# Kernel tuning notes

Hardware: AMD Instinct MI355X
Metric: run time of the kernel (lower is better)

Reference implementation:

```python
import jax, jax.numpy as jnp
import numpy as np

HEADS = 8
DIM_HEAD = 64
CHUNK = 128
EPS = 1e-6
KERNEL_EPS = 1e-4


def softmax_kernel(x, proj, is_query):
    # x: [b,h,n,d], proj: [f,d]  (FAVOR+ positive softmax features)
    d = x.shape[-1]
    data_normalizer = d ** -0.25
    ratio = proj.shape[0] ** -0.5
    data_dash = jnp.einsum('bhnd,fd->bhnf', x * data_normalizer, proj)
    diag = 0.5 * (data_normalizer ** 2) * jnp.sum(x * x, axis=-1, keepdims=True)  # [b,h,n,1]
    if is_query:
        m = jnp.max(data_dash, axis=-1, keepdims=True)
    else:
        m = jnp.max(data_dash, axis=(-1, -2), keepdims=True)
    return ratio * (jnp.exp(data_dash - diag - jax.lax.stop_gradient(m)) + KERNEL_EPS)


def infer_hidden_states(q, k, v, chunk_size=CHUNK):
    # q,k: [b,h,n,f], v: [b,h,n,e]; chunked causal linear attention with carried cumsums
    b, h, n, f = q.shape
    e = v.shape[-1]
    nc = n // chunk_size

    def to_chunks(t):
        return jnp.moveaxis(t.reshape(b, h, nc, chunk_size, t.shape[-1]), 2, 0)

    qs, ks, vs = to_chunks(q), to_chunks(k), to_chunks(v)

    def step(carry, inp):
        Z, S = carry  # [b,h,1,f], [b,h,1,f,e]
        qc, kc, vc = inp
        k_cum = Z + jnp.cumsum(kc, axis=2)                       # [b,h,c,f]
        D_inv = 1.0 / jnp.einsum('bhnf,bhnf->bhn', qc, k_cum + EPS)
        ctx = jnp.einsum('bhnf,bhne->bhnfe', kc, vc)             # [b,h,c,f,e]
        ctx_cum = S + jnp.cumsum(ctx, axis=2)
        out = jnp.einsum('bhnfe,bhnf,bhn->bhne', ctx_cum, qc, D_inv)
        return (k_cum[:, :, -1:], ctx_cum[:, :, -1:]), out

    init = (jnp.zeros((b, h, 1, f), q.dtype), jnp.zeros((b, h, 1, f, e), q.dtype))
    (Z, S), outs = jax.lax.scan(step, init, (qs, ks, vs))
    out = jnp.moveaxis(outs, 0, 2).reshape(b, h, n, e)
    return out, Z[:, :, 0], S[:, :, 0]


def reference(x, proj, Wq, Wk, Wv, Wo, bo):
    b, n, dim = x.shape
    h, dh = HEADS, DIM_HEAD

    def split_heads(t):
        return jnp.transpose(t.reshape(b, n, h, dh), (0, 2, 1, 3))

    q = split_heads(x @ Wq)
    k = split_heads(x @ Wk)
    v = split_heads(x @ Wv)

    qf = softmax_kernel(q, proj, is_query=True)
    kf = softmax_kernel(k, proj, is_query=False)

    out, Z, S = infer_hidden_states(qf, kf, v)
    out = jnp.transpose(out, (0, 2, 1, 3)).reshape(b, n, h * dh)
    out = out @ Wo + bo
    return out, Z, S


def setup_inputs() -> dict:
    key = jax.random.key(0)
    ks = jax.random.split(key, 6)
    b, n, dim = 2, 2048, 512
    f = 256
    return {
        'x': jax.random.normal(ks[0], (b, n, dim), jnp.float32),
        'proj': jax.random.normal(ks[1], (f, DIM_HEAD), jnp.float32),
        'Wq': jax.random.normal(ks[2], (dim, dim), jnp.float32) * (dim ** -0.5),
        'Wk': jax.random.normal(ks[3], (dim, dim), jnp.float32) * (dim ** -0.5),
        'Wv': jax.random.normal(ks[4], (dim, dim), jnp.float32) * (dim ** -0.5),
        'Wo': jax.random.normal(ks[5], (dim, dim), jnp.float32) * (dim ** -0.5),
        'bo': jnp.zeros((dim,), jnp.float32),
    }
```

## Files before the change

kernel.cpp:

```cpp
#include <hip/hip_runtime.h>
#include <hip/hip_bf16.h>
#include <math.h>

#define NB    2
#define NSEQ  2048
#define DIMM  512
#define NH    8
#define DHd   64
#define FF    256
#define CHK   128
#define NCHK  16
#define NBH   16

typedef unsigned short ushort_t;
typedef __attribute__((ext_vector_type(8))) __bf16 bf16x8;
typedef __attribute__((ext_vector_type(4))) float floatx4;

__device__ __forceinline__ unsigned short f2bf(float x) {
    union { __hip_bfloat16 h; unsigned short u; } v;
    v.h = __float2bfloat16(x);
    return v.u;
}
__device__ __forceinline__ float bf2f(unsigned short u) {
    union { unsigned short u2[2]; float f; } v;
    v.u2[0] = 0; v.u2[1] = u;
    return v.f;
}
__device__ __forceinline__ unsigned enc_f(float x) {
    unsigned u = __float_as_uint(x);
    return (u & 0x80000000u) ? ~u : (u | 0x80000000u);
}
__device__ __forceinline__ float dec_f(unsigned e) {
    unsigned u = (e & 0x80000000u) ? (e & 0x7fffffffu) : ~e;
    return __uint_as_float(u);
}

__device__ __forceinline__ void gload16(const void* g, void* l) {
    __builtin_amdgcn_global_load_lds(
        (const __attribute__((address_space(1))) void*)g,
        (__attribute__((address_space(3))) void*)l, 16, 0, 0);
}

__device__ __forceinline__ bf16x8 frag8(const ushort_t* lds, int row, int kb) {
    return *((const bf16x8*)lds + row * 8 + (kb ^ (row & 7)));
}
__device__ __forceinline__ bf16x8 fragS(const ushort_t* lds, int row, int kb) {
    return *((const bf16x8*)lds + row * 16 + (kb ^ (row & 15)));
}

__global__ __launch_bounds__(256)
void prep(const float* __restrict__ x, const float* __restrict__ proj,
          const float* __restrict__ W0, const float* __restrict__ W1,
          const float* __restrict__ W2, const float* __restrict__ W3,
          ushort_t* __restrict__ xb, ushort_t* __restrict__ projb,
          ushort_t* __restrict__ T0, ushort_t* __restrict__ T1,
          ushort_t* __restrict__ T2, ushort_t* __restrict__ T3,
          unsigned* __restrict__ mk_u)
{
    __shared__ float t[32][33];
    const int b = blockIdx.x, tid = threadIdx.x;
    if (b < 2048) {
        const int gid = b * 256 + tid;
        const float4 v = *(const float4*)(x + (size_t)gid * 4);
        union { ushort4 v4; unsigned short s[4]; } pk;
        pk.s[0] = f2bf(v.x); pk.s[1] = f2bf(v.y); pk.s[2] = f2bf(v.z); pk.s[3] = f2bf(v.w);
        ((ushort4*)xb)[gid] = pk.v4;
    } else if (b < 2064) {
        const int gid = (b - 2048) * 256 + tid;
        const float dn = 0.35355339059327379f;
        const float4 v = *(const float4*)(proj + (size_t)gid * 4);
        union { ushort4 v4; unsigned short s[4]; } pk;
        pk.s[0] = f2bf(v.x * dn); pk.s[1] = f2bf(v.y * dn);
        pk.s[2] = f2bf(v.z * dn); pk.s[3] = f2bf(v.w * dn);
        ((ushort4*)projb)[gid] = pk.v4;
    } else if (b < 3088) {
        const int idx = b - 2064;
        const int z = idx >> 8, rem = idx & 255;
        const int bx = rem & 15, by = rem >> 4;
        const float* W = (z == 0) ? W0 : (z == 1) ? W1 : (z == 2) ? W2 : W3;
        ushort_t* T = (z == 0) ? T0 : (z == 1) ? T1 : (z == 2) ? T2 : T3;
        const int x0 = bx * 32, y0 = by * 32;
        const int tx = tid & 31, ty = tid >> 5;
#pragma unroll
        for (int i = 0; i < 4; i++)
            t[ty + i * 8][tx] = W[(size_t)(y0 + ty + i * 8) * DIMM + x0 + tx];
        __syncthreads();
#pragma unroll
        for (int i = 0; i < 4; i++)
            T[(size_t)(x0 + ty + i * 8) * DIMM + y0 + tx] = f2bf(t[tx][ty + i * 8]);
    } else {
        if (tid < NBH) mk_u[tid] = 0u;
    }
}

__device__ __forceinline__ void mfma_mainloop(
    const ushort_t* __restrict__ AG, const ushort_t* __restrict__ BG,
    ushort_t* As, ushort_t* Bs, int ldA, int ldB, int K,
    floatx4 acc[4][4], int tid)
{
    const int lane = tid & 63, wid = tid >> 6;
    const int q = lane >> 4, c = lane & 15;
    const int wm = (wid >> 1) * 64, wn = (wid & 1) * 64;

    for (int k0 = 0; k0 < K; k0 += 64) {
#pragma unroll
        for (int t = 0; t < 4; t++) {
            const int g = t * 256 + tid, r = g >> 3, kb = (g & 7) ^ (r & 7);
            gload16(AG + (size_t)r * ldA + k0 + kb * 8, As + (size_t)g * 8);
        }
#pragma unroll
        for (int t = 0; t < 4; t++) {
            const int g = t * 256 + tid, r = g >> 3, kb = (g & 7) ^ (r & 7);
            gload16(BG + (size_t)r * ldB + k0 + kb * 8, Bs + (size_t)g * 8);
        }
        __syncthreads();
#pragma unroll
        for (int ks = 0; ks < 2; ks++) {
            bf16x8 af[4], bfr[4];
#pragma unroll
            for (int i = 0; i < 4; i++) {
                af[i]  = frag8(As, wm + i * 16 + c, ks * 4 + q);
                bfr[i] = frag8(Bs, wn + i * 16 + c, ks * 4 + q);
            }
#pragma unroll
            for (int i = 0; i < 4; i++)
#pragma unroll
                for (int j = 0; j < 4; j++)
                    acc[i][j] = __builtin_amdgcn_mfma_f32_16x16x32_bf16(
                        af[i], bfr[j], acc[i][j], 0, 0, 0);
        }
        __syncthreads();
    }
}

__global__ __launch_bounds__(256)
void gemm_qkv(const ushort_t* __restrict__ xb,
              const ushort_t* __restrict__ Wtq, const ushort_t* __restrict__ Wtk,
              const ushort_t* __restrict__ Wtv, const ushort_t* __restrict__ projb,
              ushort_t* __restrict__ qb, ushort_t* __restrict__ kb,
              ushort_t* __restrict__ vTb, unsigned* __restrict__ mk_u)
{
    __shared__ alignas(16) ushort_t SM[25600];
    __shared__ float red[256];
    ushort_t* As = SM;
    ushort_t* Bs = SM + 8192;
    ushort_t* PS = SM + 17408;
    const int tid = threadIdx.x;
    const int n0 = blockIdx.x * 128, m0 = blockIdx.y * 128, z = blockIdx.z;
    const ushort_t* Bt = (z == 0) ? Wtq : ((z == 1) ? Wtk : Wtv);

    floatx4 zero = {0.f, 0.f, 0.f, 0.f};
    floatx4 acc[4][4];
#pragma unroll
    for (int i = 0; i < 4; i++)
#pragma unroll
        for (int j = 0; j < 4; j++) acc[i][j] = zero;

    mfma_mainloop(xb + (size_t)m0 * DIMM, Bt + (size_t)n0 * DIMM, As, Bs,
                  DIMM, DIMM, DIMM, acc, tid);

    const int lane = tid & 63, wid = tid >> 6;
    const int q = lane >> 4, cl = lane & 15;
    const int wm = (wid >> 1) * 64, wn = (wid & 1) * 64;

#pragma unroll
    for (int i = 0; i < 4; i++)
#pragma unroll
        for (int j = 0; j < 4; j++) {
            const int col = wn + j * 16 + cl;
#pragma unroll
            for (int r = 0; r < 4; r++) {
                const int row = wm + i * 16 + q * 4 + r;
                SM[row * 136 + col] = f2bf(acc[i][j][r]);
            }
        }
    __syncthreads();

    if (z < 2) {
        ushort_t* ob = (z == 0) ? qb : kb;
        if (z == 1) {
#pragma unroll
            for (int t = 0; t < 4; t++) {
                const int g = t * 256 + tid, f = g >> 3, kbg = (g & 7) ^ (f & 7);
                gload16(projb + (size_t)f * 64 + kbg * 8, PS + (size_t)g * 8);
            }
        }
#pragma unroll
        for (int p = 0; p < 16; p++) {
            const int idx = p * 256 + tid;
            const int row = idx >> 5, c4 = idx & 31;
            ushort4 o = *(const ushort4*)&SM[row * 136 + c4 * 4];
            *(ushort4*)(ob + (size_t)(m0 + row) * DIMM + n0 + c4 * 4) = o;
        }
        if (z == 1) {
            const int bb = m0 >> 11;
            const int h0 = n0 >> 6;
            float mx[2] = {-3.0e38f, -3.0e38f};
#pragma unroll
            for (int half = 0; half < 2; half++) {
                __syncthreads();
#pragma unroll
                for (int hh = 0; hh < 2; hh++) {
                    floatx4 a2[4][4];
#pragma unroll
                    for (int i = 0; i < 4; i++)
#pragma unroll
                        for (int j = 0; j < 4; j++) a2[i][j] = zero;
#pragma unroll
                    for (int ks = 0; ks < 2; ks++) {
                        bf16x8 af[4], bfr[4];
#pragma unroll
                        for (int i = 0; i < 4; i++)
                            af[i] = *(const bf16x8*)&SM[(wm + i * 16 + cl) * 136 + hh * 64 + (ks * 4 + q) * 8];
#pragma unroll
                        for (int j = 0; j < 4; j++)
                            bfr[j] = frag8(PS, wn + j * 16 + cl, ks * 4 + q);
#pragma unroll
                        for (int i = 0; i < 4; i++)
#pragma unroll
                            for (int j = 0; j < 4; j++)
                                a2[i][j] = __builtin_amdgcn_mfma_f32_16x16x32_bf16(
                                    af[i], bfr[j], a2[i][j], 0, 0, 0);
                    }
#pragma unroll
                    for (int i = 0; i < 4; i++)
#pragma unroll
                        for (int j = 0; j < 4; j++)
#pragma unroll
                            for (int r = 0; r < 4; r++) mx[hh] = fmaxf(mx[hh], a2[i][j][r]);
                }
                if (half == 0) {
                    __syncthreads();
#pragma unroll
                    for (int t = 0; t < 4; t++) {
                        const int g = t * 256 + tid, f = g >> 3, kbg = (g & 7) ^ (f & 7);
                        gload16(projb + (size_t)(128 + f) * 64 + kbg * 8, PS + (size_t)g * 8);
                    }
                }
            }
#pragma unroll
            for (int hh = 0; hh < 2; hh++) {
                __syncthreads();
                red[tid] = mx[hh];
                __syncthreads();
                for (int s = 128; s > 0; s >>= 1) {
                    if (tid < s) red[tid] = fmaxf(red[tid], red[tid + s]);
                    __syncthreads();
                }
                if (tid == 0) atomicMax(&mk_u[bb * NH + h0 + hh], enc_f(red[0]));
            }
        }
    } else {
        const int bb = m0 >> 11, nbase = m0 & 2047;
#pragma unroll
        for (int p = 0; p < 16; p++) {
            const int idx = p * 256 + tid;
            const int cl2 = idx >> 5, n4 = idx & 31;
            const int C = n0 + cl2;
            const int h = C >> 6, e = C & 63;
            union { ushort4 v4; unsigned short s[4]; } pk;
#pragma unroll
            for (int k = 0; k < 4; k++) pk.s[k] = SM[(n4 * 4 + k) * 136 + cl2];
            *(ushort4*)(vTb + (((size_t)(bb * NH + h) * 64 + e)) * NSEQ + nbase + n4 * 4) = pk.v4;
        }
    }
}

__global__ __launch_bounds__(256)
void gemm_out(const ushort_t* __restrict__ attnb, const ushort_t* __restrict__ Wto,
              float* __restrict__ out, const float* __restrict__ bias)
{
    __shared__ alignas(16) ushort_t As[8192];
    __shared__ alignas(16) ushort_t Bs[8192];
    const int tid = threadIdx.x;
    const int n0 = blockIdx.x * 128, m0 = blockIdx.y * 128;

    floatx4 zero = {0.f, 0.f, 0.f, 0.f};
    floatx4 acc[4][4];
#pragma unroll
    for (int i = 0; i < 4; i++)
#pragma unroll
        for (int j = 0; j < 4; j++) acc[i][j] = zero;

    mfma_mainloop(attnb + (size_t)m0 * DIMM, Wto + (size_t)n0 * DIMM, As, Bs,
                  DIMM, DIMM, DIMM, acc, tid);

    const int lane = tid & 63, wid = tid >> 6;
    const int q = lane >> 4, c = lane & 15;
    const int wm = (wid >> 1) * 64, wn = (wid & 1) * 64;
#pragma unroll
    for (int i = 0; i < 4; i++)
#pragma unroll
        for (int j = 0; j < 4; j++) {
            const int col = n0 + wn + j * 16 + c;
            const float bv = bias[col];
#pragma unroll
            for (int r = 0; r < 4; r++) {
                const int row = m0 + wm + i * 16 + q * 4 + r;
                out[(size_t)row * DIMM + col] = acc[i][j][r] + bv;
            }
        }
}

__global__ __launch_bounds__(256)
void featk(const ushort_t* __restrict__ kb_, const ushort_t* __restrict__ projb,
           const unsigned* __restrict__ mk_u, const ushort_t* __restrict__ vTb,
           ushort_t* __restrict__ kfb, float* __restrict__ CTXT,
           float* __restrict__ Ksum)
{
    __shared__ alignas(16) ushort_t SM[24576];
    __shared__ float dtmp[256];
    __shared__ float diag_l[128];
    __shared__ float colp[2][256];
    ushort_t* As = SM;
    ushort_t* Bs = SM + 8192;
    const int tid = threadIdx.x, lane = tid & 63, wid = tid >> 6;
    const int q = lane >> 4, cl = lane & 15;
    const int m0 = blockIdx.x * 128, h = blockIdx.y;
    const int bb = m0 >> 11, nloc = m0 & 2047;
    const int bh = bb * NH + h;
    const int cidx = nloc >> 7;
    const ushort_t* Aq = kb_ + (size_t)m0 * DIMM + h * 64;

    {
        const int row = tid >> 1, half = tid & 1;
        float s = 0.f;
        const ushort_t* p = Aq + (size_t)row * DIMM + half * 32;
#pragma unroll
        for (int d = 0; d < 32; d += 4) {
            ushort4 w = *(const ushort4*)(p + d);
            float a = bf2f(w.x), b2 = bf2f(w.y), c2 = bf2f(w.z), d2 = bf2f(w.w);
            s += a * a + b2 * b2 + c2 * c2 + d2 * d2;
        }
        dtmp[tid] = s;
    }
    __syncthreads();
    if (tid < 128) diag_l[tid] = (dtmp[2 * tid] + dtmp[2 * tid + 1]) * 0.0625f;

#pragma unroll
    for (int t = 0; t < 4; t++) {
        const int g = t * 256 + tid, r = g >> 3, kb = (g & 7) ^ (r & 7);
        gload16(Aq + (size_t)r * DIMM + kb * 8, As + (size_t)g * 8);
    }
#pragma unroll
    for (int t = 0; t < 8; t++) {
        const int g = t * 256 + tid, r = g >> 3, kb = (g & 7) ^ (r & 7);
        gload16(projb + (size_t)r * 64 + kb * 8, Bs + (size_t)g * 8);
    }
    __syncthreads();

    floatx4 zero = {0.f, 0.f, 0.f, 0.f};
    floatx4 acc[4][8];
#pragma unroll
    for (int i = 0; i < 4; i++)
#pragma unroll
        for (int j = 0; j < 8; j++) acc[i][j] = zero;
    const int wm = (wid >> 1) * 64, wn = (wid & 1) * 128;
#pragma unroll
    for (int ks = 0; ks < 2; ks++) {
        bf16x8 af[4], bfr[8];
#pragma unroll
        for (int i = 0; i < 4; i++) af[i] = frag8(As, wm + i * 16 + cl, ks * 4 + q);
#pragma unroll
        for (int j = 0; j < 8; j++) bfr[j] = frag8(Bs, wn + j * 16 + cl, ks * 4 + q);
#pragma unroll
        for (int i = 0; i < 4; i++)
#pragma unroll
            for (int j = 0; j < 8; j++)
                acc[i][j] = __builtin_amdgcn_mfma_f32_16x16x32_bf16(
                    af[i], bfr[j], acc[i][j], 0, 0, 0);
    }
    __syncthreads();

    const float mk = dec_f(mk_u[bh]);
#pragma unroll
    for (int i = 0; i < 4; i++)
#pragma unroll
        for (int r = 0; r < 4; r++) {
            const int row = wm + i * 16 + q * 4 + r;
            const float cc = diag_l[row] + mk;
#pragma unroll
            for (int j = 0; j < 8; j++)
                acc[i][j][r] = 0.0625f * (__expf(acc[i][j][r] - cc) + 1.0e-4f);
        }

#pragma unroll
    for (int j = 0; j < 8; j++) {
        float s = 0.f;
#pragma unroll
        for (int i = 0; i < 4; i++)
            s += acc[i][j][0] + acc[i][j][1] + acc[i][j][2] + acc[i][j][3];
        s += __shfl_xor(s, 16);
        s += __shfl_xor(s, 32);
        if (q == 0) colp[wid >> 1][wn + j * 16 + cl] = s;
    }

    const size_t frow = (size_t)bh * NSEQ + nloc;
#pragma unroll
    for (int hf = 0; hf < 2; hf++) {
        __syncthreads();
        if ((wid & 1) == hf) {
#pragma unroll
            for (int i = 0; i < 4; i++)
#pragma unroll
                for (int j = 0; j < 8; j++) {
                    const int col = j * 16 + cl;
#pragma unroll
                    for (int r = 0; r < 4; r++) {
                        const int row = wm + i * 16 + q * 4 + r;
                        SM[row * 132 + col] = f2bf(acc[i][j][r]);
                    }
                }
        }
        if (hf == 0) {
            Ksum[((size_t)bh * NCHK + cidx) * FF + tid] = colp[0][tid] + colp[1][tid];
        }
        __syncthreads();
#pragma unroll
        for (int p = 0; p < 16; p++) {
            const int idx = p * 256 + tid;
            const int row = idx >> 5, c4 = idx & 31;
            ushort4 o = *(const ushort4*)&SM[row * 132 + c4 * 4];
            *(ushort4*)(kfb + (frow + row) * FF + hf * 128 + c4 * 4) = o;
        }
    }

    __syncthreads();
    ushort_t* Vs = SM;
    ushort_t* T  = SM + 8192;
    const ushort_t* Vg = vTb + ((size_t)bh * 64) * NSEQ + nloc;
#pragma unroll
    for (int t = 0; t < 4; t++) {
        const int g = t * 256 + tid, r = g >> 4, kb = (g & 15) ^ (r & 15);
        gload16(Vg + (size_t)r * NSEQ + kb * 8, Vs + (size_t)g * 8);
    }

    const size_t cbase = ((size_t)bh * NCHK + cidx) * 64;
#pragma unroll
    for (int fq = 0; fq < 4; fq++) {
        if ((wid & 1) == (fq >> 1)) {
#pragma unroll
            for (int jj = 0; jj < 4; jj++) {
                const int j = (fq & 1) * 4 + jj;
#pragma unroll
                for (int i = 0; i < 4; i++)
#pragma unroll
                    for (int r = 0; r < 4; r++) {
                        const int n = wm + i * 16 + q * 4 + r;
                        T[(jj * 16 + cl) * 136 + n] = f2bf(acc[i][j][r]);
                    }
            }
        }
        __syncthreads();
        floatx4 accc[4];
#pragma unroll
        for (int jj = 0; jj < 4; jj++) accc[jj] = zero;
#pragma unroll
        for (int kt = 0; kt < 4; kt++) {
            const bf16x8 av = fragS(Vs, wid * 16 + cl, kt * 4 + q);
#pragma unroll
            for (int jj = 0; jj < 4; jj++) {
                const bf16x8 bv = *(const bf16x8*)(T + (jj * 16 + cl) * 136 + (kt * 4 + q) * 8);
                accc[jj] = __builtin_amdgcn_mfma_f32_16x16x32_bf16(av, bv, accc[jj], 0, 0, 0);
            }
        }
#pragma unroll
        for (int jj = 0; jj < 4; jj++) {
            const int f = fq * 64 + jj * 16 + cl;
#pragma unroll
            for (int r = 0; r < 4; r++) {
                const int e = wid * 16 + q * 4 + r;
                CTXT[(cbase + e) * FF + f] = accc[jj][r];
            }
        }
        __syncthreads();
    }
}

__global__ void prefix_zs(float* __restrict__ Ksum, float* __restrict__ Zout,
                          const float* __restrict__ CTXT, ushort_t* __restrict__ ctxp,
                          float* __restrict__ Sout)
{
    const int b = blockIdx.x;
    if (b < 1024) {
        const int idx = b * 256 + threadIdx.x;
        const int bh = idx >> 14, ef = idx & 16383;
        const int e = ef >> 8, f = ef & 255;
        float run = 0.f;
#pragma unroll
        for (int c = 0; c < NCHK; c++) {
            const size_t o = (((size_t)bh * NCHK + c) * 64 + e) * FF + f;
            const float t = CTXT[o];
            ctxp[o] = f2bf(run);
            run += t;
        }
        Sout[((size_t)bh * FF + f) * 64 + e] = run;
    } else {
        const int idx = (b - 1024) * 256 + threadIdx.x;
        const int bh = idx >> 8, f = idx & 255;
        float run = 0.f;
#pragma unroll
        for (int c = 0; c < NCHK; c++) {
            const size_t o = ((size_t)(bh * NCHK + c)) * FF + f;
            const float t = Ksum[o];
            Ksum[o] = run;
            run += t;
        }
        Zout[(size_t)bh * FF + f] = run;
    }
}

__global__ __launch_bounds__(256)
void chunk_out_mfma(const ushort_t* __restrict__ qb_, const ushort_t* __restrict__ projb,
                    const ushort_t* __restrict__ kfb, const ushort_t* __restrict__ vTb,
                    const float* __restrict__ Zex, const ushort_t* __restrict__ ctxp,
                    ushort_t* __restrict__ attnb)
{
    __shared__ alignas(16) ushort_t QF[32768];
    __shared__ alignas(16) ushort_t Sld[16384];
    __shared__ alignas(16) ushort_t As[8192];
    __shared__ alignas(16) ushort_t Bs[8192];
    __shared__ float zeps[256];
    __shared__ float rows_part[2][128];
    __shared__ float denp[256];
    __shared__ float den_l[128];
    __shared__ float dtmp[256];
    __shared__ float diag_l[128];
    __shared__ float mx2[2][128];

    const int tid = threadIdx.x, lane = tid & 63, wid = tid >> 6;
    const int q = lane >> 4, cl = lane & 15;
    const int bh = blockIdx.x >> 4, c = blockIdx.x & 15;
    const int bb = bh >> 3, h = bh & 7;
    const int n0 = c * CHK;
    const ushort_t* Kf = kfb + ((size_t)bh * NSEQ + n0) * FF;
    const ushort_t* Aq = qb_ + ((size_t)(bb * NSEQ + n0)) * DIMM + h * 64;

    zeps[tid] = Zex[((size_t)bh * NCHK + c) * FF + tid] + 1.0e-6f;

    {
        const int row = tid >> 1, half = tid & 1;
        float s = 0.f;
        const ushort_t* p = Aq + (size_t)row * DIMM + half * 32;
#pragma unroll
        for (int d = 0; d < 32; d += 4) {
            ushort4 w = *(const ushort4*)(p + d);
            float a = bf2f(w.x), b2 = bf2f(w.y), c2 = bf2f(w.z), d2 = bf2f(w.w);
            s += a * a + b2 * b2 + c2 * c2 + d2 * d2;
        }
        dtmp[tid] = s;
    }
    __syncthreads();
    if (tid < 128) diag_l[tid] = (dtmp[2 * tid] + dtmp[2 * tid + 1]) * 0.0625f;

#pragma unroll
    for (int t = 0; t < 4; t++) {
        const int g = t * 256 + tid, r = g >> 3, kb = (g & 7) ^ (r & 7);
        gload16(Aq + (size_t)r * DIMM + kb * 8, As + (size_t)g * 8);
    }
#pragma unroll
    for (int t = 0; t < 8; t++) {
        const int g = t * 256 + tid, r = g >> 3, kb = (g & 7) ^ (r & 7);
        gload16(projb + (size_t)r * 64 + kb * 8, Sld + (size_t)g * 8);
    }
    __syncthreads();

    floatx4 zero = {0.f, 0.f, 0.f, 0.f};
    {
        floatx4 accq[4][8];
#pragma unroll
        for (int i = 0; i < 4; i++)
#pragma unroll
            for (int j = 0; j < 8; j++) accq[i][j] = zero;
        const int wmF = (wid >> 1) * 64, wnF = (wid & 1) * 128;
#pragma unroll
        for (int ks = 0; ks < 2; ks++) {
            bf16x8 af[4], bfr[8];
#pragma unroll
            for (int i = 0; i < 4; i++) af[i] = frag8(As, wmF + i * 16 + cl, ks * 4 + q);
#pragma unroll
            for (int j = 0; j < 8; j++) bfr[j] = frag8(Sld, wnF + j * 16 + cl, ks * 4 + q);
#pragma unroll
            for (int i = 0; i < 4; i++)
#pragma unroll
                for (int j = 0; j < 8; j++)
                    accq[i][j] = __builtin_amdgcn_mfma_f32_16x16x32_bf16(
                        af[i], bfr[j], accq[i][j], 0, 0, 0);
        }
#pragma unroll
        for (int i = 0; i < 4; i++)
#pragma unroll
            for (int r = 0; r < 4; r++) {
                const int row = wmF + i * 16 + q * 4 + r;
                float mx = -3.0e38f;
#pragma unroll
                for (int j = 0; j < 8; j++) mx = fmaxf(mx, accq[i][j][r]);
                mx = fmaxf(mx, __shfl_xor(mx, 1)); mx = fmaxf(mx, __shfl_xor(mx, 2));
                mx = fmaxf(mx, __shfl_xor(mx, 4)); mx = fmaxf(mx, __shfl_xor(mx, 8));
                if (cl == 0) mx2[wid & 1][row] = mx;
            }
        __syncthreads();
#pragma unroll
        for (int i = 0; i < 4; i++)
#pragma unroll
            for (int r = 0; r < 4; r++) {
                const int row = wmF + i * 16 + q * 4 + r;
                const float cc = diag_l[row] + fmaxf(mx2[0][row], mx2[1][row]);
#pragma unroll
                for (int j = 0; j < 8; j++) {
                    const int col = wnF + j * 16 + cl;
                    const float v = 0.0625f * (__expf(accq[i][j][r] - cc) + 1.0e-4f);
                    const int s = col >> 6, fp = col & 63;
                    QF[s * 8192 + (row * 8 + ((fp >> 3) ^ (row & 7))) * 8 + (fp & 7)] = f2bf(v);
                }
            }
    }
    __syncthreads();

    floatx4 acc1[4][4];
#pragma unroll
    for (int i = 0; i < 4; i++)
#pragma unroll
        for (int j = 0; j < 4; j++) acc1[i][j] = zero;
    const int wm = (wid >> 1) * 64, wn = (wid & 1) * 64;
    for (int k0 = 0; k0 < FF; k0 += 64) {
#pragma unroll
        for (int t = 0; t < 4; t++) {
            const int g = t * 256 + tid, r = g >> 3, kb = (g & 7) ^ (r & 7);
            gload16(Kf + (size_t)r * FF + k0 + kb * 8, Bs + (size_t)g * 8);
        }
        __syncthreads();
        const ushort_t* QFs = QF + (k0 >> 6) * 8192;
#pragma unroll
        for (int ks = 0; ks < 2; ks++) {
            bf16x8 af[4], bfr[4];
#pragma unroll
            for (int i = 0; i < 4; i++) {
                af[i]  = frag8(QFs, wm + i * 16 + cl, ks * 4 + q);
                bfr[i] = frag8(Bs, wn + i * 16 + cl, ks * 4 + q);
            }
#pragma unroll
            for (int i = 0; i < 4; i++)
#pragma unroll
                for (int j = 0; j < 4; j++)
                    acc1[i][j] = __builtin_amdgcn_mfma_f32_16x16x32_bf16(
                        af[i], bfr[j], acc1[i][j], 0, 0, 0);
        }
        __syncthreads();
    }
#pragma unroll
    for (int i = 0; i < 4; i++)
#pragma unroll
        for (int r = 0; r < 4; r++) {
            const int row = wm + i * 16 + q * 4 + r;
            float part = 0.f;
#pragma unroll
            for (int j = 0; j < 4; j++) {
                const int col = wn + j * 16 + cl;
                const float v = (col <= row) ? acc1[i][j][r] : 0.f;
                part += v;
                Sld[(row * 16 + ((col >> 3) ^ (row & 15))) * 8 + (col & 7)] = f2bf(v);
            }
            part += __shfl_xor(part, 1); part += __shfl_xor(part, 2);
            part += __shfl_xor(part, 4); part += __shfl_xor(part, 8);
            if (cl == 0) rows_part[wid & 1][row] = part;
        }
    __syncthreads();

    floatx4 acc2[4][2];
#pragma unroll
    for (int i = 0; i < 4; i++)
#pragma unroll
        for (int j = 0; j < 2; j++) acc2[i][j] = zero;
    const ushort_t* Vt = vTb + ((size_t)bh * 64) * NSEQ + n0;
    for (int k0 = 0; k0 < CHK; k0 += 64) {
#pragma unroll
        for (int t = 0; t < 2; t++) {
            const int g = t * 256 + tid, r = g >> 3, kb = (g & 7) ^ (r & 7);
            gload16(Vt + (size_t)r * NSEQ + k0 + kb * 8, As + (size_t)g * 8);
        }
        __syncthreads();
#pragma unroll
        for (int ks = 0; ks < 2; ks++) {
            bf16x8 af[4], bfr[2];
            const int kbS = (k0 >> 3) + ks * 4 + q;
#pragma unroll
            for (int i = 0; i < 4; i++) af[i] = frag8(As, i * 16 + cl, ks * 4 + q);
#pragma unroll
            for (int j = 0; j < 2; j++) bfr[j] = fragS(Sld, wid * 32 + j * 16 + cl, kbS);
#pragma unroll
            for (int i = 0; i < 4; i++)
#pragma unroll
                for (int j = 0; j < 2; j++)
                    acc2[i][j] = __builtin_amdgcn_mfma_f32_16x16x32_bf16(
                        af[i], bfr[j], acc2[i][j], 0, 0, 0);
        }
        __syncthreads();
    }

    const ushort_t* Cp = ctxp + ((size_t)bh * NCHK + c) * 64 * FF;
    float dacc = 0.f;
    const int drow = tid & 127, dhalf = tid >> 7;
    for (int k0 = 0; k0 < FF; k0 += 64) {
#pragma unroll
        for (int t = 0; t < 2; t++) {
            const int g = t * 256 + tid, r = g >> 3, kb = (g & 7) ^ (r & 7);
            gload16(Cp + (size_t)r * FF + k0 + kb * 8, As + (size_t)g * 8);
        }
        __syncthreads();
        const ushort_t* QFs = QF + (k0 >> 6) * 8192;
#pragma unroll
        for (int ks = 0; ks < 2; ks++) {
            bf16x8 af[4], bfr[2];
#pragma unroll
            for (int i = 0; i < 4; i++) af[i] = frag8(As, i * 16 + cl, ks * 4 + q);
#pragma unroll
            for (int j = 0; j < 2; j++) bfr[j] = frag8(QFs, wid * 32 + j * 16 + cl, ks * 4 + q);
#pragma unroll
            for (int i = 0; i < 4; i++)
#pragma unroll
                for (int j = 0; j < 2; j++)
                    acc2[i][j] = __builtin_amdgcn_mfma_f32_16x16x32_bf16(
                        af[i], bfr[j], acc2[i][j], 0, 0, 0);
        }
#pragma unroll
        for (int gi = 0; gi < 4; gi++) {
            const int kb = dhalf * 4 + gi;
            const ushort_t* gp = QFs + ((size_t)drow * 8 + (kb ^ (drow & 7))) * 8;
            const int kbase = k0 + kb * 8;
#pragma unroll
            for (int e2 = 0; e2 < 8; e2++)
                dacc = fmaf(bf2f(gp[e2]), zeps[kbase + e2], dacc);
        }
        __syncthreads();
    }
    denp[tid] = dacc;
    __syncthreads();
    if (tid < 128)
        den_l[tid] = rows_part[0][tid] + rows_part[1][tid] + denp[tid] + denp[tid + 128];
    __syncthreads();

#pragma unroll
    for (int j = 0; j < 2; j++) {
        const int row = wid * 32 + j * 16 + cl;
        const float dinv = 1.0f / den_l[row];
#pragma unroll
        for (int i = 0; i < 4; i++)
#pragma unroll
            for (int r = 0; r < 4; r++) {
                const int e = i * 16 + q * 4 + r;
                Sld[row * 68 + e] = f2bf(acc2[i][j][r] * dinv);
            }
    }
    __syncthreads();
#pragma unroll
    for (int p = 0; p < 8; p++) {
        const int idx = p * 256 + tid;
        const int row = idx >> 4, e4 = idx & 15;
        ushort4 o = *(const ushort4*)&Sld[row * 68 + e4 * 4];
        *(ushort4*)(attnb + ((size_t)(bb * NSEQ + n0 + row)) * DIMM + h * 64 + e4 * 4) = o;
    }
}

extern "C" void kernel_launch(void* const* d_in, const int* in_sizes, int n_in,
                              void* d_out, int out_size, void* d_ws, size_t ws_size,
                              hipStream_t stream)
{
    (void)in_sizes; (void)n_in; (void)out_size; (void)ws_size;
    const float* x    = (const float*)d_in[0];
    const float* proj = (const float*)d_in[1];
    const float* Wq   = (const float*)d_in[2];
    const float* Wk   = (const float*)d_in[3];
    const float* Wv   = (const float*)d_in[4];
    const float* Wo   = (const float*)d_in[5];
    const float* bo   = (const float*)d_in[6];
    float* out = (float*)d_out;

    char* W = (char*)d_ws;
    float*    CTXT = (float*)W;              W += (size_t)16777216;
    ushort_t* kfb  = (ushort_t*)W;           W += (size_t)16777216;
    ushort_t* ctxp = (ushort_t*)W;           W += (size_t)8388608;
    ushort_t* qb   = (ushort_t*)W;           W += (size_t)4194304;
    ushort_t* kb   = (ushort_t*)W;           W += (size_t)4194304;
    ushort_t* xb   = (ushort_t*)W;           W += (size_t)4194304;
    ushort_t* vTb  = (ushort_t*)W;           W += (size_t)4194304;
    ushort_t* Wtq  = (ushort_t*)W;           W += (size_t)524288;
    ushort_t* Wtk  = (ushort_t*)W;           W += (size_t)524288;
    ushort_t* Wtv  = (ushort_t*)W;           W += (size_t)524288;
    ushort_t* Wto  = (ushort_t*)W;           W += (size_t)524288;
    ushort_t* projb = (ushort_t*)W;          W += (size_t)32768;
    float*    Ksum = (float*)W;              W += (size_t)262144;
    unsigned* mk_u = (unsigned*)W;           W += (size_t)256;

    ushort_t* attnb = xb;

    float* Zout = out + (size_t)4096 * 512;
    float* Sout = Zout + (size_t)NBH * FF;

    hipLaunchKernelGGL(prep, dim3(3089), dim3(256), 0, stream,
                       x, proj, Wq, Wk, Wv, Wo, xb, projb, Wtq, Wtk, Wtv, Wto, mk_u);
    hipLaunchKernelGGL(gemm_qkv, dim3(4, 32, 3), dim3(256), 0, stream,
                       xb, Wtq, Wtk, Wtv, projb, qb, kb, vTb, mk_u);
    hipLaunchKernelGGL(featk, dim3(32, 8), dim3(256), 0, stream,
                       kb, projb, mk_u, vTb, kfb, CTXT, Ksum);
    hipLaunchKernelGGL(prefix_zs, dim3(1040), dim3(256), 0, stream,
                       Ksum, Zout, CTXT, ctxp, Sout);
    hipLaunchKernelGGL(chunk_out_mfma, dim3(256), dim3(256), 0, stream,
                       qb, projb, kfb, vTb, Ksum, ctxp, attnb);
    hipLaunchKernelGGL(gemm_out, dim3(4, 32), dim3(256), 0, stream, attnb, Wto, out, bo);
}
```

Measured before the change: 149.6 us.

## Recompute key features in chunk kernel instead of storing them to global memory

The featk kernel no longer writes the bf16 key feature matrix (kfb, 16 MB buffer) to global memory. chunk_out_mfma now reloads the raw key slice, recomputes the key feature map with an extra MFMA GEMM and exp pass, and keeps it in one enlarged shared-memory buffer for the intra-chunk QK^T product. This removes a large global write and read round trip and the per-k-step loads with their barriers. In exchange it duplicates feature computation and raises LDS use per block to about 128 KB plus scratch, which can cut occupancy.

```diff
diff --git a/kernel.cpp b/kernel.cpp
--- a/kernel.cpp
+++ b/kernel.cpp
@@ -305,8 +305,7 @@
 __global__ __launch_bounds__(256)
 void featk(const ushort_t* __restrict__ kb_, const ushort_t* __restrict__ projb,
            const unsigned* __restrict__ mk_u, const ushort_t* __restrict__ vTb,
-           ushort_t* __restrict__ kfb, float* __restrict__ CTXT,
-           float* __restrict__ Ksum)
+           float* __restrict__ CTXT, float* __restrict__ Ksum)
 {
     __shared__ alignas(16) ushort_t SM[24576];
     __shared__ float dtmp[256];
@@ -394,38 +393,9 @@
         s += __shfl_xor(s, 32);
         if (q == 0) colp[wid >> 1][wn + j * 16 + cl] = s;
     }
-
-    const size_t frow = (size_t)bh * NSEQ + nloc;
-#pragma unroll
-    for (int hf = 0; hf < 2; hf++) {
-        __syncthreads();
-        if ((wid & 1) == hf) {
-#pragma unroll
-            for (int i = 0; i < 4; i++)
-#pragma unroll
-                for (int j = 0; j < 8; j++) {
-                    const int col = j * 16 + cl;
-#pragma unroll
-                    for (int r = 0; r < 4; r++) {
-                        const int row = wm + i * 16 + q * 4 + r;
-                        SM[row * 132 + col] = f2bf(acc[i][j][r]);
-                    }
-                }
-        }
-        if (hf == 0) {
-            Ksum[((size_t)bh * NCHK + cidx) * FF + tid] = colp[0][tid] + colp[1][tid];
-        }
-        __syncthreads();
-#pragma unroll
-        for (int p = 0; p < 16; p++) {
-            const int idx = p * 256 + tid;
-            const int row = idx >> 5, c4 = idx & 31;
-            ushort4 o = *(const ushort4*)&SM[row * 132 + c4 * 4];
-            *(ushort4*)(kfb + (frow + row) * FF + hf * 128 + c4 * 4) = o;
-        }
-    }
-
-    __syncthreads();
+    __syncthreads();
+    Ksum[((size_t)bh * NCHK + cidx) * FF + tid] = colp[0][tid] + colp[1][tid];
+
     ushort_t* Vs = SM;
     ushort_t* T  = SM + 8192;
     const ushort_t* Vg = vTb + ((size_t)bh * 64) * NSEQ + nloc;
@@ -511,21 +481,19 @@
 }
 
 __global__ __launch_bounds__(256)
-void chunk_out_mfma(const ushort_t* __restrict__ qb_, const ushort_t* __restrict__ projb,
-                    const ushort_t* __restrict__ kfb, const ushort_t* __restrict__ vTb,
+void chunk_out_mfma(const ushort_t* __restrict__ qb_, const ushort_t* __restrict__ kb_,
+                    const ushort_t* __restrict__ projb, const ushort_t* __restrict__ vTb,
                     const float* __restrict__ Zex, const ushort_t* __restrict__ ctxp,
-                    ushort_t* __restrict__ attnb)
+                    const unsigned* __restrict__ mk_u, ushort_t* __restrict__ attnb)
 {
-    __shared__ alignas(16) ushort_t QF[32768];
-    __shared__ alignas(16) ushort_t Sld[16384];
-    __shared__ alignas(16) ushort_t As[8192];
-    __shared__ alignas(16) ushort_t Bs[8192];
+    __shared__ alignas(16) ushort_t SMX[65536];
     __shared__ float zeps[256];
     __shared__ float rows_part[2][128];
     __shared__ float denp[256];
     __shared__ float den_l[128];
     __shared__ float dtmp[256];
     __shared__ float diag_l[128];
+    __shared__ float diagk_l[128];
     __shared__ float mx2[2][128];
 
     const int tid = threadIdx.x, lane = tid & 63, wid = tid >> 6;
@@ -533,11 +501,26 @@
     const int bh = blockIdx.x >> 4, c = blockIdx.x & 15;
     const int bb = bh >> 3, h = bh & 7;
     const int n0 = c * CHK;
-    const ushort_t* Kf = kfb + ((size_t)bh * NSEQ + n0) * FF;
     const ushort_t* Aq = qb_ + ((size_t)(bb * NSEQ + n0)) * DIMM + h * 64;
+    const ushort_t* Ak = kb_ + ((size_t)(bb * NSEQ + n0)) * DIMM + h * 64;
 
     zeps[tid] = Zex[((size_t)bh * NCHK + c) * FF + tid] + 1.0e-6f;
 
+#pragma unroll
+    for (int t = 0; t < 4; t++) {
+        const int g = t * 256 + tid, r = g >> 3, kb2 = (g & 7) ^ (r & 7);
+        gload16(Aq + (size_t)r * DIMM + kb2 * 8, SMX + 16384 + (size_t)g * 8);
+    }
+#pragma unroll
+    for (int t = 0; t < 4; t++) {
+        const int g = t * 256 + tid, r = g >> 3, kb2 = (g & 7) ^ (r & 7);
+        gload16(Ak + (size_t)r * DIMM + kb2 * 8, SMX + 24576 + (size_t)g * 8);
+    }
+#pragma unroll
+    for (int t = 0; t < 8; t++) {
+        const int g = t * 256 + tid, r = g >> 3, kb2 = (g & 7) ^ (r & 7);
+        gload16(projb + (size_t)r * 64 + kb2 * 8, SMX + (size_t)g * 8);
+    }
     {
         const int row = tid >> 1, half = tid & 1;
         float s = 0.f;
@@ -552,34 +535,40 @@
     }
     __syncthreads();
     if (tid < 128) diag_l[tid] = (dtmp[2 * tid] + dtmp[2 * tid + 1]) * 0.0625f;
-
-#pragma unroll
-    for (int t = 0; t < 4; t++) {
-        const int g = t * 256 + tid, r = g >> 3, kb = (g & 7) ^ (r & 7);
-        gload16(Aq + (size_t)r * DIMM + kb * 8, As + (size_t)g * 8);
-    }
-#pragma unroll
-    for (int t = 0; t < 8; t++) {
-        const int g = t * 256 + tid, r = g >> 3, kb = (g & 7) ^ (r & 7);
-        gload16(projb + (size_t)r * 64 + kb * 8, Sld + (size_t)g * 8);
-    }
-    __syncthreads();
-
+    __syncthreads();
+    {
+        const int row = tid >> 1, half = tid & 1;
+        float s = 0.f;
+        const ushort_t* p = Ak + (size_t)row * DIMM + half * 32;
+#pragma unroll
+        for (int d = 0; d < 32; d += 4) {
+            ushort4 w = *(const ushort4*)(p + d);
+            float a = bf2f(w.x), b2 = bf2f(w.y), c2 = bf2f(w.z), d2 = bf2f(w.w);
+            s += a * a + b2 * b2 + c2 * c2 + d2 * d2;
+        }
+        dtmp[tid] = s;
+    }
+    __syncthreads();
+    if (tid < 128) diagk_l[tid] = (dtmp[2 * tid] + dtmp[2 * tid + 1]) * 0.0625f;
+    __syncthreads();
+
+    const float mk = dec_f(mk_u[bh]);
     floatx4 zero = {0.f, 0.f, 0.f, 0.f};
+    const int wmF = (wid >> 1) * 64, wnF = (wid & 1) * 128;
+
     {
         floatx4 accq[4][8];
 #pragma unroll
         for (int i = 0; i < 4; i++)
 #pragma unroll
             for (int j = 0; j < 8; j++) accq[i][j] = zero;
-        const int wmF = (wid >> 1) * 64, wnF = (wid & 1) * 128;
 #pragma unroll
         for (int ks = 0; ks < 2; ks++) {
             bf16x8 af[4], bfr[8];
 #pragma unroll
-            for (int i = 0; i < 4; i++) af[i] = frag8(As, wmF + i * 16 + cl, ks * 4 + q);
-#pragma unroll
-            for (int j = 0; j < 8; j++) bfr[j] = frag8(Sld, wnF + j * 16 + cl, ks * 4 + q);
+            for (int i = 0; i < 4; i++) af[i] = frag8(SMX + 16384, wmF + i * 16 + cl, ks * 4 + q);
+#pragma unroll
+            for (int j = 0; j < 8; j++) bfr[j] = frag8(SMX, wnF + j * 16 + cl, ks * 4 + q);
 #pragma unroll
             for (int i = 0; i < 4; i++)
 #pragma unroll
@@ -611,7 +600,52 @@
                     const int col = wnF + j * 16 + cl;
                     const float v = 0.0625f * (__expf(accq[i][j][r] - cc) + 1.0e-4f);
                     const int s = col >> 6, fp = col & 63;
-                    QF[s * 8192 + (row * 8 + ((fp >> 3) ^ (row & 7))) * 8 + (fp & 7)] = f2bf(v);
+                    SMX[32768 + s * 8192 + ((size_t)row * 8 + ((fp >> 3) ^ (row & 7))) * 8 + (fp & 7)] = f2bf(v);
+                }
+            }
+    }
+
+    {
+        floatx4 acck[4][8];
+#pragma unroll
+        for (int i = 0; i < 4; i++)
+#pragma unroll
+            for (int j = 0; j < 8; j++) acck[i][j] = zero;
+#pragma unroll
+        for (int ks = 0; ks < 2; ks++) {
+            bf16x8 af[4], bfr[8];
+#pragma unroll
+            for (int i = 0; i < 4; i++) af[i] = frag8(SMX + 24576, wmF + i * 16 + cl, ks * 4 + q);
+#pragma unroll
+            for (int j = 0; j < 8; j++) bfr[j] = frag8(SMX, wnF + j * 16 + cl, ks * 4 + q);
+#pragma unroll
+            for (int i = 0; i < 4; i++)
+#pragma unroll
+                for (int j = 0; j < 8; j++)
+                    acck[i][j] = __builtin_amdgcn_mfma_f32_16x16x32_bf16(
+                        af[i], bfr[j], acck[i][j], 0, 0, 0);
+        }
+#pragma unroll
+        for (int i = 0; i < 4; i++)
+#pragma unroll
+            for (int r = 0; r < 4; r++) {
+                const int row = wmF + i * 16 + q * 4 + r;
+                const float cc = diagk_l[row] + mk;
+#pragma unroll
+                for (int j = 0; j < 8; j++)
+                    acck[i][j][r] = 0.0625f * (__expf(acck[i][j][r] - cc) + 1.0e-4f);
+            }
+        __syncthreads();
+#pragma unroll
+        for (int i = 0; i < 4; i++)
+#pragma unroll
+            for (int r = 0; r < 4; r++) {
+                const int row = wmF + i * 16 + q * 4 + r;
+#pragma unroll
+                for (int j = 0; j < 8; j++) {
+                    const int col = wnF + j * 16 + cl;
+                    const int s = col >> 6, fp = col & 63;
+                    SMX[s * 8192 + ((size_t)row * 8 + ((fp >> 3) ^ (row & 7))) * 8 + (fp & 7)] = f2bf(acck[i][j][r]);
                 }
             }
     }
@@ -623,21 +657,17 @@
 #pragma unroll
         for (int j = 0; j < 4; j++) acc1[i][j] = zero;
     const int wm = (wid >> 1) * 64, wn = (wid & 1) * 64;
-    for (int k0 = 0; k0 < FF; k0 += 64) {
-#pragma unroll
-        for (int t = 0; t < 4; t++) {
-            const int g = t * 256 + tid, r = g >> 3, kb = (g & 7) ^ (r & 7);
-            gload16(Kf + (size_t)r * FF + k0 + kb * 8, Bs + (size_t)g * 8);
-        }
-        __syncthreads();
-        const ushort_t* QFs = QF + (k0 >> 6) * 8192;
+#pragma unroll
+    for (int s = 0; s < 4; s++) {
+        const ushort_t* QFs = SMX + 32768 + s * 8192;
+        const ushort_t* KFs = SMX + s * 8192;
 #pragma unroll
         for (int ks = 0; ks < 2; ks++) {
             bf16x8 af[4], bfr[4];
 #pragma unroll
             for (int i = 0; i < 4; i++) {
                 af[i]  = frag8(QFs, wm + i * 16 + cl, ks * 4 + q);
-                bfr[i] = frag8(Bs, wn + i * 16 + cl, ks * 4 + q);
+                bfr[i] = frag8(KFs, wn + i * 16 + cl, ks * 4 + q);
             }
 #pragma unroll
             for (int i = 0; i < 4; i++)
@@ -646,8 +676,9 @@
                     acc1[i][j] = __builtin_amdgcn_mfma_f32_16x16x32_bf16(
                         af[i], bfr[j], acc1[i][j], 0, 0, 0);
         }
-        __syncthreads();
-    }
+    }
+    __syncthreads();
+
 #pragma unroll
     for (int i = 0; i < 4; i++)
 #pragma unroll
@@ -659,7 +690,7 @@
                 const int col = wn + j * 16 + cl;
                 const float v = (col <= row) ? acc1[i][j][r] : 0.f;
                 part += v;
-                Sld[(row * 16 + ((col >> 3) ^ (row & 15))) * 8 + (col & 7)] = f2bf(v);
+                SMX[((size_t)row * 16 + ((col >> 3) ^ (row & 15))) * 8 + (col & 7)] = f2bf(v);
             }
             part += __shfl_xor(part, 1); part += __shfl_xor(part, 2);
             part += __shfl_xor(part, 4); part += __shfl_xor(part, 8);
@@ -676,8 +707,8 @@
     for (int k0 = 0; k0 < CHK; k0 += 64) {
 #pragma unroll
         for (int t = 0; t < 2; t++) {
-            const int g = t * 256 + tid, r = g >> 3, kb = (g & 7) ^ (r & 7);
-            gload16(Vt + (size_t)r * NSEQ + k0 + kb * 8, As + (size_t)g * 8);
+            const int g = t * 256 + tid, r = g >> 3, kb2 = (g & 7) ^ (r & 7);
+            gload16(Vt + (size_t)r * NSEQ + k0 + kb2 * 8, SMX + 16384 + (size_t)g * 8);
         }
         __syncthreads();
 #pragma unroll
@@ -685,9 +716,9 @@
             bf16x8 af[4], bfr[2];
             const int kbS = (k0 >> 3) + ks * 4 + q;
 #pragma unroll
-            for (int i = 0; i < 4; i++) af[i] = frag8(As, i * 16 + cl, ks * 4 + q);
-#pragma unroll
-            for (int j = 0; j < 2; j++) bfr[j] = fragS(Sld, wid * 32 + j * 16 + cl, kbS);
+            for (int i = 0; i < 4; i++) af[i] = frag8(SMX + 16384, i * 16 + cl, ks * 4 + q);
+#pragma unroll
+            for (int j = 0; j < 2; j++) bfr[j] = fragS(SMX, wid * 32 + j * 16 + cl, kbS);
 #pragma unroll
             for (int i = 0; i < 4; i++)
 #pragma unroll
@@ -704,16 +735,16 @@
     for (int k0 = 0; k0 < FF; k0 += 64) {
 #pragma unroll
         for (int t = 0; t < 2; t++) {
-            const int g = t * 256 + tid, r = g >> 3, kb = (g & 7) ^ (r & 7);
-            gload16(Cp + (size_t)r * FF + k0 + kb * 8, As + (size_t)g * 8);
-        }
-        __syncthreads();
-        const ushort_t* QFs = QF + (k0 >> 6) * 8192;
+            const int g = t * 256 + tid, r = g >> 3, kb2 = (g & 7) ^ (r & 7);
+            gload16(Cp + (size_t)r * FF + k0 + kb2 * 8, SMX + 16384 + (size_t)g * 8);
+        }
+        __syncthreads();
+        const ushort_t* QFs = SMX + 32768 + (k0 >> 6) * 8192;
 #pragma unroll
         for (int ks = 0; ks < 2; ks++) {
             bf16x8 af[4], bfr[2];
 #pragma unroll
-            for (int i = 0; i < 4; i++) af[i] = frag8(As, i * 16 + cl, ks * 4 + q);
+            for (int i = 0; i < 4; i++) af[i] = frag8(SMX + 16384, i * 16 + cl, ks * 4 + q);
 #pragma unroll
             for (int j = 0; j < 2; j++) bfr[j] = frag8(QFs, wid * 32 + j * 16 + cl, ks * 4 + q);
 #pragma unroll
@@ -725,9 +756,9 @@
         }
 #pragma unroll
         for (int gi = 0; gi < 4; gi++) {
-            const int kb = dhalf * 4 + gi;
-            const ushort_t* gp = QFs + ((size_t)drow * 8 + (kb ^ (drow & 7))) * 8;
-            const int kbase = k0 + kb * 8;
+            const int kb2 = dhalf * 4 + gi;
+            const ushort_t* gp = QFs + ((size_t)drow * 8 + (kb2 ^ (drow & 7))) * 8;
+            const int kbase = k0 + kb2 * 8;
 #pragma unroll
             for (int e2 = 0; e2 < 8; e2++)
                 dacc = fmaf(bf2f(gp[e2]), zeps[kbase + e2], dacc);
@@ -749,7 +780,7 @@
 #pragma unroll
             for (int r = 0; r < 4; r++) {
                 const int e = i * 16 + q * 4 + r;
-                Sld[row * 68 + e] = f2bf(acc2[i][j][r] * dinv);
+                SMX[row * 68 + e] = f2bf(acc2[i][j][r] * dinv);
             }
     }
     __syncthreads();
@@ -757,7 +788,7 @@
     for (int p = 0; p < 8; p++) {
         const int idx = p * 256 + tid;
         const int row = idx >> 4, e4 = idx & 15;
-        ushort4 o = *(const ushort4*)&Sld[row * 68 + e4 * 4];
+        ushort4 o = *(const ushort4*)&SMX[row * 68 + e4 * 4];
         *(ushort4*)(attnb + ((size_t)(bb * NSEQ + n0 + row)) * DIMM + h * 64 + e4 * 4) = o;
     }
 }
@@ -778,7 +809,6 @@
 
     char* W = (char*)d_ws;
     float*    CTXT = (float*)W;              W += (size_t)16777216;
-    ushort_t* kfb  = (ushort_t*)W;           W += (size_t)16777216;
     ushort_t* ctxp = (ushort_t*)W;           W += (size_t)8388608;
     ushort_t* qb   = (ushort_t*)W;           W += (size_t)4194304;
     ushort_t* kb   = (ushort_t*)W;           W += (size_t)4194304;
@@ -802,10 +832,10 @@
     hipLaunchKernelGGL(gemm_qkv, dim3(4, 32, 3), dim3(256), 0, stream,
                        xb, Wtq, Wtk, Wtv, projb, qb, kb, vTb, mk_u);
     hipLaunchKernelGGL(featk, dim3(32, 8), dim3(256), 0, stream,
-                       kb, projb, mk_u, vTb, kfb, CTXT, Ksum);
+                       kb, projb, mk_u, vTb, CTXT, Ksum);
     hipLaunchKernelGGL(prefix_zs, dim3(1040), dim3(256), 0, stream,
                        Ksum, Zout, CTXT, ctxp, Sout);
     hipLaunchKernelGGL(chunk_out_mfma, dim3(256), dim3(256), 0, stream,
-                       qb, projb, kfb, vTb, Ksum, ctxp, attnb);
+                       qb, kb, projb, vTb, Ksum, ctxp, mk_u, attnb);
     hipLaunchKernelGGL(gemm_out, dim3(4, 32), dim3(256), 0, stream, attnb, Wto, out, bo);
 }
```

Result: slower. 177.1 us (+18.4%).
